# Performance work log

Measured on AMD Instinct MI355X. Metric: run time of the kernel, lower is better.

## Reference

```python
import jax, jax.numpy as jnp
import numpy as np


def setup_inputs() -> dict:
    key = jax.random.key(0)
    k1, k2 = jax.random.split(key)
    N_KV, MAX_CTX, HEAD_DIM, CHUNK = 8, 32768, 128, 2048
    k_cache = jnp.zeros((1, N_KV, MAX_CTX, HEAD_DIM), dtype=jnp.float32)
    v_cache = jnp.zeros((1, N_KV, MAX_CTX, HEAD_DIM), dtype=jnp.float32)
    pos_ids = jnp.arange(CHUNK, dtype=jnp.int64)
    k = jax.random.normal(k1, (1, N_KV, CHUNK, HEAD_DIM), dtype=jnp.float32)
    v = jax.random.normal(k2, (1, N_KV, CHUNK, HEAD_DIM), dtype=jnp.float32)
    return {"k_cache": k_cache, "v_cache": v_cache, "pos_ids": pos_ids, "k": k, "v": v}


def reference(k_cache, v_cache, pos_ids, k, v):
    # kout[:, :, pos_ids, :] = k  (scatter write along the context axis)
    kout = k_cache.at[:, :, pos_ids, :].set(k)
    vout = v_cache.at[:, :, pos_ids, :].set(v)
    return (kout, vout)
```

## Files before the change

### kernel.cpp

```cpp
#include <hip/hip_runtime.h>


typedef float v4f __attribute__((ext_vector_type(4)));

constexpr int  N_KV     = 8;
constexpr int  MAX_CTX  = 32768;
constexpr int  HEAD_DIM = 128;
constexpr int  CHUNK    = 2048;

constexpr long CACHE_ELEMS = (long)N_KV * MAX_CTX * HEAD_DIM;
constexpr long CACHE_N4    = CACHE_ELEMS / 4;
constexpr int  C4          = HEAD_DIM / 4;

__global__ void inv_init_kernel(int* __restrict__ inv) {
    int i = blockIdx.x * blockDim.x + threadIdx.x;
    if (i < MAX_CTX) inv[i] = -1;
}

__global__ void inv_fill_kernel(const int* __restrict__ pos, int* __restrict__ inv) {
    int j = blockIdx.x * blockDim.x + threadIdx.x;
    if (j < CHUNK) inv[pos[j]] = j;
}

__global__ void kv_fused_kernel(const v4f* __restrict__ kc,
                                const v4f* __restrict__ vc,
                                const v4f* __restrict__ k,
                                const v4f* __restrict__ v,
                                const int* __restrict__ inv,
                                v4f* __restrict__ out_k,
                                v4f* __restrict__ out_v) {
    long i = (long)blockIdx.x * blockDim.x + threadIdx.x;
    if (i >= CACHE_N4) return;
    int  col = (int)(i & (C4 - 1));
    long r   = i >> 5;
    int  row = (int)(r & (MAX_CTX - 1));
    int  h   = (int)(r >> 15);
    int  j   = inv[row];

    v4f a, b;
    if (j >= 0) {
        long s = ((long)h * CHUNK + j) * C4 + col;
        a = k[s];
        b = v[s];
    } else {
        a = __builtin_nontemporal_load(&kc[i]);
        b = __builtin_nontemporal_load(&vc[i]);
    }
    __builtin_nontemporal_store(a, &out_k[i]);
    __builtin_nontemporal_store(b, &out_v[i]);
}

extern "C" void kernel_launch(void* const* d_in, const int* in_sizes, int n_in,
                              void* d_out, int out_size, void* d_ws, size_t ws_size,
                              hipStream_t stream) {
    const v4f* k_cache = (const v4f*)d_in[0];
    const v4f* v_cache = (const v4f*)d_in[1];
    const int* pos     = (const int*)d_in[2];
    const v4f* k       = (const v4f*)d_in[3];
    const v4f* v       = (const v4f*)d_in[4];

    float* out   = (float*)d_out;
    v4f*   out_k = (v4f*)out;
    v4f*   out_v = (v4f*)(out + CACHE_ELEMS);

    int* inv = (int*)d_ws;

    inv_init_kernel<<<MAX_CTX / 256, 256, 0, stream>>>(inv);
    inv_fill_kernel<<<CHUNK / 256, 256, 0, stream>>>(pos, inv);

    {
        int  block = 256;
        long grid  = (CACHE_N4 + block - 1) / block;
        kv_fused_kernel<<<(int)grid, block, 0, stream>>>(k_cache, v_cache, k, v,
                                                         inv, out_k, out_v);
    }
}
```

Baseline: 456.8 us.

## Replace inverse-map fused kernel with full cache copy plus direct scatter

Removes the inverse-index construction kernels and the per-element inv lookup. The cache is now copied wholesale in one kernel, then a second kernel scatters k/v rows to their pos locations. The rows later overwritten by the scatter are still read and written during the copy, so there is redundant traffic. The change also drops the nontemporal load/store hints, relies on launch ordering for correctness, and reads pos as int even though it is int64.

```diff
diff --git a/kernel.cpp b/kernel.cpp
--- a/kernel.cpp
+++ b/kernel.cpp
@@ -10,44 +10,32 @@
 
 constexpr long CACHE_ELEMS = (long)N_KV * MAX_CTX * HEAD_DIM;
 constexpr long CACHE_N4    = CACHE_ELEMS / 4;
+constexpr long KV_N4       = (long)N_KV * CHUNK * HEAD_DIM/4;
 constexpr int  C4          = HEAD_DIM / 4;
 
-__global__ void inv_init_kernel(int* __restrict__ inv) {
-    int i = blockIdx.x * blockDim.x + threadIdx.x;
-    if (i < MAX_CTX) inv[i] = -1;
+__global__ void kv_copy_kernel(const v4f* __restrict__ kc,
+                               const v4f* __restrict__ vc,
+                               v4f* __restrict__ out_k,
+                               v4f* __restrict__ out_v) {
+    long i = (long)blockIdx.x * blockDim.x + threadIdx.x;
+    out_k[i] = kc[i];
+    out_v[i] = vc[i];
 }
 
-__global__ void inv_fill_kernel(const int* __restrict__ pos, int* __restrict__ inv) {
-    int j = blockIdx.x * blockDim.x + threadIdx.x;
-    if (j < CHUNK) inv[pos[j]] = j;
-}
-
-__global__ void kv_fused_kernel(const v4f* __restrict__ kc,
-                                const v4f* __restrict__ vc,
-                                const v4f* __restrict__ k,
-                                const v4f* __restrict__ v,
-                                const int* __restrict__ inv,
-                                v4f* __restrict__ out_k,
-                                v4f* __restrict__ out_v) {
-    long i = (long)blockIdx.x * blockDim.x + threadIdx.x;
-    if (i >= CACHE_N4) return;
+__global__ void kv_scatter_kernel(const v4f* __restrict__ k,
+                                  const v4f* __restrict__ v,
+                                  const int* __restrict__ pos,
+                                  v4f* __restrict__ out_k,
+                                  v4f* __restrict__ out_v) {
+    long i   = (long)blockIdx.x * blockDim.x + threadIdx.x;
     int  col = (int)(i & (C4 - 1));
     long r   = i >> 5;
-    int  row = (int)(r & (MAX_CTX - 1));
-    int  h   = (int)(r >> 15);
-    int  j   = inv[row];
-
-    v4f a, b;
-    if (j >= 0) {
-        long s = ((long)h * CHUNK + j) * C4 + col;
-        a = k[s];
-        b = v[s];
-    } else {
-        a = __builtin_nontemporal_load(&kc[i]);
-        b = __builtin_nontemporal_load(&vc[i]);
-    }
-    __builtin_nontemporal_store(a, &out_k[i]);
-    __builtin_nontemporal_store(b, &out_v[i]);
+    int  row = (int)(r & (CHUNK - 1));
+    int  h   = (int)(r >> 11);
+    long p   = (long)pos[row];
+    long o   = ((long)h * MAX_CTX + p) * C4 + col;
+    out_k[o] = k[i];
+    out_v[o] = v[i];
 }
 
 extern "C" void kernel_launch(void* const* d_in, const int* in_sizes, int n_in,
@@ -63,15 +51,8 @@
     v4f*   out_k = (v4f*)out;
     v4f*   out_v = (v4f*)(out + CACHE_ELEMS);
 
-    int* inv = (int*)d_ws;
-
-    inv_init_kernel<<<MAX_CTX / 256, 256, 0, stream>>>(inv);
-    inv_fill_kernel<<<CHUNK / 256, 256, 0, stream>>>(pos, inv);
-
-    {
-        int  block = 256;
-        long grid  = (CACHE_N4 + block - 1) / block;
-        kv_fused_kernel<<<(int)grid, block, 0, stream>>>(k_cache, v_cache, k, v,
-                                                         inv, out_k, out_v);
-    }
+    kv_copy_kernel<<<(int)(CACHE_N4 / 256), 256, 0, stream>>>(k_cache, v_cache,
+                                                              out_k, out_v);
+    kv_scatter_kernel<<<(int)(KV_N4 / 256), 256, 0, stream>>>(k, v, pos,
+                                                              out_k, out_v);
 }
```

Result: no change. 448.1 us (-1.9%).
